# Kernel tuning notes

Hardware: AMD Instinct MI355X
Metric: run time of the kernel (lower is better)

The kernel has to match this reference:

```python
import jax, jax.numpy as jnp
import numpy as np

B, T, C = 2, 2048, 1024
H = 16
HD = C // H  # 64


def setup_inputs() -> dict:
    key = jax.random.key(0)
    k1, k2, k3, k4, k5 = jax.random.split(key, 5)
    s = 0.02
    return {
        "x": jax.random.normal(k1, (B, T, C), dtype=jnp.float32),
        "w_attn": jax.random.normal(k2, (C, 3 * C), dtype=jnp.float32) * s,
        "b_attn": jnp.zeros((3 * C,), dtype=jnp.float32),
        "w_proj": jax.random.normal(k3, (C, C), dtype=jnp.float32) * s,
        "b_proj": jnp.zeros((C,), dtype=jnp.float32),
    }


def reference(x, w_attn, b_attn, w_proj, b_proj):
    Bx, Tx, Cx = x.shape
    qkv = x @ w_attn + b_attn                      # [B,T,3C]
    q, k, v = jnp.split(qkv, 3, axis=-1)
    # [B,T,C] -> [B,H,T,HD]
    def heads(t):
        return t.reshape(Bx, Tx, H, HD).transpose(0, 2, 1, 3)
    q, k, v = heads(q), heads(k), heads(v)
    scale = 1.0 / np.sqrt(HD).astype(np.float32)
    scores = jnp.einsum("bhqd,bhkd->bhqk", q, k) * scale
    causal = jnp.tril(jnp.ones((Tx, Tx), dtype=bool))
    scores = jnp.where(causal, scores, -jnp.inf)
    attn = jax.nn.softmax(scores, axis=-1)          # dropout p=0 -> identity
    y = jnp.einsum("bhqk,bhkd->bhqd", attn, v)
    y = y.transpose(0, 2, 1, 3).reshape(Bx, Tx, Cx)
    return y @ w_proj + b_proj
```

## Files before the change

kernel.cpp:

```cpp
#include <hip/hip_runtime.h>
#include <hip/hip_bf16.h>

#define Bb 2
#define Tt 2048
#define Cc 1024
#define Hh 16
#define HD 64
#define QS 0.18033688f

typedef __attribute__((ext_vector_type(8))) short bf16x8;
typedef __attribute__((ext_vector_type(4))) short bf16x4;
typedef __attribute__((ext_vector_type(4))) float f32x4;
typedef __attribute__((ext_vector_type(2))) unsigned int u32x2;

__device__ inline short f2b(float f) {
    unsigned int u = __builtin_bit_cast(unsigned int, f);
    unsigned int r = (u + 0x7FFFu + ((u >> 16) & 1u)) >> 16;
    return (short)(unsigned short)r;
}

__device__ inline void gl16(const void* g, void* l) {
    __builtin_amdgcn_global_load_lds(
        (const __attribute__((address_space(1))) void*)g,
        (__attribute__((address_space(3))) void*)l, 16, 0, 0);
}

__global__ __launch_bounds__(256) void prep_kernel(
    const float* __restrict__ x, short* __restrict__ xbf,
    const float* __restrict__ wA, short* __restrict__ wAT,
    const float* __restrict__ wP, short* __restrict__ wPT)
{
    const int bx = blockIdx.x, tid = threadIdx.x;
    if (bx < 2048) {
        int i = (bx * 256 + tid) * 8;
        float4 a = *(const float4*)(x + i);
        float4 b = *(const float4*)(x + i + 4);
        bf16x8 v;
        v[0] = f2b(a.x); v[1] = f2b(a.y); v[2] = f2b(a.z); v[3] = f2b(a.w);
        v[4] = f2b(b.x); v[5] = f2b(b.y); v[6] = f2b(b.z); v[7] = f2b(b.w);
        *(bf16x8*)(xbf + i) = v;
        return;
    }
    const float* W; short* WT; int N, t;
    if (bx < 2816) { t = bx - 2048; W = wA; WT = wAT; N = 3072; }
    else           { t = bx - 2816; W = wP; WT = wPT; N = 1024; }
    const int K = 1024;
    int k0 = (t & 15) * 64, n0 = (t >> 4) * 64;
    int nl = tid & 63, kg = tid >> 6;
    int n = n0 + nl;
    short v[16];
#pragma unroll
    for (int i = 0; i < 16; i++)
        v[i] = f2b(W[(size_t)(k0 + kg * 16 + i) * N + n]);
    short* dst = WT + (size_t)n * K + k0 + kg * 16;
    *(bf16x8*)dst = *(bf16x8*)&v[0];
    *(bf16x8*)(dst + 8) = *(bf16x8*)&v[8];
}

#define VM4 asm volatile("s_waitcnt vmcnt(4)" ::: "memory")
#define VM2 asm volatile("s_waitcnt vmcnt(2)" ::: "memory")
#define VM0 asm volatile("s_waitcnt vmcnt(0)" ::: "memory")
#define VMN (void)0
#define BARRIER asm volatile("s_barrier" ::: "memory")

#define STG_A(nb, h, kb) { \
    gl16(A + baA[h] + (kb), &LB[(((nb) << 1) | (h)) * 8192 + dst8]); \
    gl16(A + baA[h] + 131072 + (kb), &LB[(((nb) << 1) | (h)) * 8192 + dst8 + 4096]); }
#define STG_B(nb, h, kb) { \
    gl16(Bt + baB[h] + (kb), &LB[32768 + (((nb) << 1) | (h)) * 8192 + dst8]); \
    gl16(Bt + baB[h] + 131072 + (kb), &LB[32768 + (((nb) << 1) | (h)) * 8192 + dst8 + 4096]); }

#define PHASE(bb, MH, NH, STG, WAIT) { \
    WAIT; \
    BARRIER; \
    const short* Ab_ = &LB[(((bb) << 1) | (MH)) * 8192]; \
    const short* Bb_ = &LB[32768 + (((bb) << 1) | (NH)) * 8192]; \
    bf16x8 af_[4][2], bf_[2][2]; \
    _Pragma("unroll") for (int f_ = 0; f_ < 4; f_++) \
        _Pragma("unroll") for (int kh_ = 0; kh_ < 2; kh_++) \
            af_[f_][kh_] = *(const bf16x8*)&Ab_[aro[f_] + kx[kh_]]; \
    _Pragma("unroll") for (int e_ = 0; e_ < 2; e_++) \
        _Pragma("unroll") for (int kh_ = 0; kh_ < 2; kh_++) \
            bf_[e_][kh_] = *(const bf16x8*)&Bb_[bro[e_] + kx[kh_]]; \
    STG; \
    __builtin_amdgcn_s_setprio(1); \
    _Pragma("unroll") for (int f_ = 0; f_ < 4; f_++) \
        _Pragma("unroll") for (int e_ = 0; e_ < 2; e_++) \
            _Pragma("unroll") for (int kh_ = 0; kh_ < 2; kh_++) \
                acc[(MH) * 4 + f_][(NH) * 2 + e_] = \
                    __builtin_amdgcn_mfma_f32_16x16x32_bf16( \
                        af_[f_][kh_], bf_[e_][kh_], \
                        acc[(MH) * 4 + f_][(NH) * 2 + e_], 0, 0, 0); \
    __builtin_amdgcn_s_setprio(0); }

__global__ __launch_bounds__(512, 2) void gemm_qkv(
    const short* __restrict__ A, const short* __restrict__ Bt,
    const float* __restrict__ bias,
    short* __restrict__ qw, short* __restrict__ kw, short* __restrict__ vTw,
    int M, int N, int K)
{
    __shared__ __attribute__((aligned(16))) short LB[65536];

    const int tid  = threadIdx.x;
    const int wave = tid >> 6, lane = tid & 63;
    const int quad = lane >> 4, lr = lane & 15;
    const int wm = wave >> 2, wn = wave & 3;

    const int bid = blockIdx.x;
    const int sw = (bid & 7) * 24 + (bid >> 3);
    const int bx = sw % 12, by = sw / 12;
    const int m0 = by * 256, n0 = bx * 256;

    const int dst8 = tid * 8;
    size_t baA[2], baB[2];
    {
        int r = tid >> 3;
        int cs = ((tid & 7) ^ (r & 7)) << 3;
#pragma unroll
        for (int h = 0; h < 2; h++) {
            int gA = m0 + ((r >> 6) << 7) + h * 64 + (r & 63);
            int gB = n0 + ((r >> 5) << 6) + h * 32 + (r & 31);
            baA[h] = (size_t)gA * 1024 + cs;
            baB[h] = (size_t)gB * 1024 + cs;
        }
    }

    int aro[4], bro[2], kx[2];
#pragma unroll
    for (int f = 0; f < 4; f++) aro[f] = (wm * 64 + f * 16 + lr) * 64;
#pragma unroll
    for (int e = 0; e < 2; e++) bro[e] = (wn * 32 + e * 16 + lr) * 64;
#pragma unroll
    for (int kh = 0; kh < 2; kh++)
        kx[kh] = (((kh * 4 + quad) ^ (lr & 7)) << 3);

    f32x4 acc[8][4];
    const f32x4 zf = {0.f, 0.f, 0.f, 0.f};
#pragma unroll
    for (int mf = 0; mf < 8; mf++)
#pragma unroll
        for (int nf = 0; nf < 4; nf++) acc[mf][nf] = zf;

    STG_A(0, 0, 0); STG_B(0, 0, 0); STG_A(0, 1, 0); STG_B(0, 1, 0);

    for (int t = 0; t < 15; ++t) {
        const int bb = t & 1, nb = bb ^ 1;
        const int kb1 = (t + 1) << 6;
        PHASE(bb, 0, 0, STG_A(nb, 0, kb1), VM4);
        PHASE(bb, 1, 0, STG_B(nb, 0, kb1), VM4);
        PHASE(bb, 0, 1, STG_A(nb, 1, kb1), VM4);
        PHASE(bb, 1, 1, STG_B(nb, 1, kb1), VMN);
    }
    PHASE(1, 0, 0, VMN, VM4);
    PHASE(1, 1, 0, VMN, VM2);
    PHASE(1, 0, 1, VMN, VM0);
    PHASE(1, 1, 1, VMN, VMN);

    if (n0 < 2048) {
#pragma unroll
        for (int nf = 0; nf < 4; nf++) {
            int c = n0 + wn * 64 + nf * 16 + lr;
            float bv = bias[c];
            int which = c >> 10, cc = c & 1023;
            int h = cc >> 6, d = cc & 63;
            short* base = which ? kw : qw;
            float qs = which ? 1.0f : QS;
#pragma unroll
            for (int mf = 0; mf < 8; mf++)
#pragma unroll
                for (int r = 0; r < 4; r++) {
                    int rg = m0 + wm * 128 + mf * 16 + quad * 4 + r;
                    int b = rg >> 11, tq = rg & 2047;
                    float val = acc[mf][nf][r] + bv;
                    base[(((size_t)b * Hh + h) * Tt + tq) * HD + d] = f2b(val * qs);
                }
        }
    } else {
#pragma unroll
        for (int p = 0; p < 2; p++) {
            __syncthreads();
            if ((wn >> 1) == p) {
#pragma unroll
                for (int nf = 0; nf < 4; nf++) {
                    int cl = (wn & 1) * 64 + nf * 16 + lr;
                    float bv = bias[n0 + p * 128 + cl];
#pragma unroll
                    for (int mf = 0; mf < 8; mf++)
#pragma unroll
                        for (int r = 0; r < 4; r++) {
                            int tl = wm * 128 + mf * 16 + quad * 4 + r;
                            LB[cl * 264 + tl] = f2b(acc[mf][nf][r] + bv);
                        }
                }
            }
            __syncthreads();
            const int rl = tid >> 2, seg = tid & 3;
            const int cc = (n0 & 1023) + p * 128 + rl;
            const int h = cc >> 6, d = cc & 63;
            const int b2 = m0 >> 11, tb = (m0 & 2047) + seg * 64;
            short* dstv = vTw + (((size_t)b2 * Hh + h) * HD + d) * Tt + tb;
            const short* srcv = &LB[rl * 264 + seg * 64];
#pragma unroll
            for (int jj = 0; jj < 8; jj++)
                *(bf16x8*)(dstv + jj * 8) = *(const bf16x8*)(srcv + jj * 8);
        }
    }
}

__global__ __launch_bounds__(256) void gemm_proj(
    const short* __restrict__ A, const short* __restrict__ Bt,
    const float* __restrict__ bias, float* __restrict__ out,
    int M, int N, int K)
{
    __shared__ __attribute__((aligned(16))) short SH[12288];

    const int tid  = threadIdx.x;
    const int wave = tid >> 6, lane = tid & 63;
    const int quad = lane >> 4, lr = lane & 15;
    const int wm = wave >> 1, wn = wave & 1;
    const int m0 = blockIdx.y * 64, n0 = blockIdx.x * 128;

    const int arow = tid >> 2;
    const int acol = ((tid & 3) ^ ((arow >> 1) & 3)) << 3;
    int brow[2], bcol[2];
#pragma unroll
    for (int i = 0; i < 2; i++) {
        int id = i * 256 + tid;
        brow[i] = id >> 2;
        bcol[i] = ((id & 3) ^ ((brow[i] >> 1) & 3)) << 3;
    }
    const int pfrag = quad ^ ((lr >> 1) & 3);

    f32x4 acc[2][4];
    const f32x4 zf = {0.f, 0.f, 0.f, 0.f};
#pragma unroll
    for (int mi = 0; mi < 2; mi++)
#pragma unroll
        for (int ni = 0; ni < 4; ni++) acc[mi][ni] = zf;

    auto asrc = [&](int row, int col) -> const short* {
        int rg = m0 + row, b = rg >> 11, t = rg & 2047;
        int h = col >> 6, d = col & 63;
        return A + ((((size_t)b * Hh + h) * Tt + t) * HD + d);
    };

    gl16(asrc(arow, acol), &SH[tid * 8]);
#pragma unroll
    for (int i = 0; i < 2; i++)
        gl16(Bt + (size_t)(n0 + brow[i]) * K + bcol[i],
             &SH[4096 + (i * 256 + tid) * 8]);

    const int iters = K >> 5;
    for (int it = 0; it < iters; ++it) {
        const int coA = (it & 1) * 2048, noA = ((it & 1) ^ 1) * 2048;
        const int coB = (it & 1) * 4096, noB = ((it & 1) ^ 1) * 4096;
        __syncthreads();
        if (it + 1 < iters) {
            const int k1 = (it + 1) << 5;
            gl16(asrc(arow, k1 + acol), &SH[noA + tid * 8]);
#pragma unroll
            for (int i = 0; i < 2; i++)
                gl16(Bt + (size_t)(n0 + brow[i]) * K + k1 + bcol[i],
                     &SH[4096 + noB + (i * 256 + tid) * 8]);
        }
        bf16x8 af[2], bf[4];
#pragma unroll
        for (int mi = 0; mi < 2; mi++) {
            int row = wm * 32 + mi * 16 + lr;
            af[mi] = *(bf16x8*)&SH[coA + (row * 4 + pfrag) * 8];
        }
#pragma unroll
        for (int ni = 0; ni < 4; ni++) {
            int row = wn * 64 + ni * 16 + lr;
            bf[ni] = *(bf16x8*)&SH[4096 + coB + (row * 4 + pfrag) * 8];
        }
#pragma unroll
        for (int mi = 0; mi < 2; mi++)
#pragma unroll
            for (int ni = 0; ni < 4; ni++)
                acc[mi][ni] = __builtin_amdgcn_mfma_f32_16x16x32_bf16(
                    af[mi], bf[ni], acc[mi][ni], 0, 0, 0);
    }

#pragma unroll
    for (int mi = 0; mi < 2; mi++)
#pragma unroll
        for (int ni = 0; ni < 4; ni++) {
            int c = n0 + wn * 64 + ni * 16 + lr;
            float bv = bias[c];
#pragma unroll
            for (int r = 0; r < 4; r++) {
                int rg = m0 + wm * 32 + mi * 16 + quad * 4 + r;
                out[(size_t)rg * N + c] = acc[mi][ni][r] + bv;
            }
        }
}

__global__ __launch_bounds__(256) void gemm_f32src(
    const void* __restrict__ Araw, const float* __restrict__ Bm,
    const float* __restrict__ bias, float* __restrict__ out,
    short* __restrict__ qw, short* __restrict__ kw, short* __restrict__ vTw,
    int M, int N, int K, int mode)
{
    __shared__ __attribute__((aligned(16))) short As[128 * 32];
    __shared__ __attribute__((aligned(16))) short Bs[128 * 32];

    const int tid  = threadIdx.x;
    const int wave = tid >> 6, lane = tid & 63;
    const int quad = lane >> 4, lr = lane & 15;
    const int wm = wave >> 1, wn = wave & 1;
    const int m0 = blockIdx.y * 128, n0 = blockIdx.x * 128;

    f32x4 acc[4][4];
    const f32x4 zf = {0.f, 0.f, 0.f, 0.f};
#pragma unroll
    for (int mi = 0; mi < 4; mi++)
#pragma unroll
        for (int ni = 0; ni < 4; ni++) acc[mi][ni] = zf;

    for (int k0 = 0; k0 < K; k0 += 32) {
        __syncthreads();
        if (mode == 1) {
            const float* Af = (const float*)Araw;
#pragma unroll
            for (int i = 0; i < 4; i++) {
                int id  = i * 256 + tid;
                int row = id >> 3;
                int kc  = (id & 7) << 2;
                float4 v = *(const float4*)(Af + (size_t)(m0 + row) * K + k0 + kc);
                short* d = &As[row * 32 + kc];
                d[0] = f2b(v.x); d[1] = f2b(v.y); d[2] = f2b(v.z); d[3] = f2b(v.w);
            }
        } else {
            const short* Ah = (const short*)Araw;
#pragma unroll
            for (int i = 0; i < 2; i++) {
                int id  = i * 256 + tid;
                int row = id >> 2;
                int kc  = (id & 3) << 3;
                int rg = m0 + row, b = rg >> 11, t = rg & 2047;
                int c = k0 + kc, h = c >> 6, d = c & 63;
                *(bf16x8*)&As[row * 32 + kc] =
                    *(const bf16x8*)(Ah + ((((size_t)b * Hh + h) * Tt + t) * HD + d));
            }
        }
#pragma unroll
        for (int i = 0; i < 4; i++) {
            int id = i * 256 + tid;
            int kr = id >> 5;
            int nc = (id & 31) << 2;
            float4 v = *(const float4*)(Bm + (size_t)(k0 + kr) * N + n0 + nc);
            Bs[(nc + 0) * 32 + kr] = f2b(v.x);
            Bs[(nc + 1) * 32 + kr] = f2b(v.y);
            Bs[(nc + 2) * 32 + kr] = f2b(v.z);
            Bs[(nc + 3) * 32 + kr] = f2b(v.w);
        }
        __syncthreads();

        bf16x8 af[4], bf[4];
#pragma unroll
        for (int mi = 0; mi < 4; mi++)
            af[mi] = *(bf16x8*)&As[(wm * 64 + mi * 16 + lr) * 32 + quad * 8];
#pragma unroll
        for (int ni = 0; ni < 4; ni++)
            bf[ni] = *(bf16x8*)&Bs[(wn * 64 + ni * 16 + lr) * 32 + quad * 8];
#pragma unroll
        for (int mi = 0; mi < 4; mi++)
#pragma unroll
            for (int ni = 0; ni < 4; ni++)
                acc[mi][ni] = __builtin_amdgcn_mfma_f32_16x16x32_bf16(
                    af[mi], bf[ni], acc[mi][ni], 0, 0, 0);
    }

#pragma unroll
    for (int mi = 0; mi < 4; mi++) {
#pragma unroll
        for (int ni = 0; ni < 4; ni++) {
            int c = n0 + wn * 64 + ni * 16 + lr;
            float bv = bias[c];
#pragma unroll
            for (int r = 0; r < 4; r++) {
                int rg = m0 + wm * 64 + mi * 16 + quad * 4 + r;
                float val = acc[mi][ni][r] + bv;
                if (mode == 1) {
                    int which = c >> 10, cc = c & 1023;
                    int h = cc >> 6, d = cc & 63;
                    int b = rg >> 11, t = rg & 2047;
                    size_t bh = (size_t)b * Hh + h;
                    if (which == 0)      qw[(bh * Tt + t) * HD + d] = f2b(val * QS);
                    else if (which == 1) kw[(bh * Tt + t) * HD + d] = f2b(val);
                    else                 vTw[(bh * HD + d) * Tt + t] = f2b(val);
                } else {
                    out[(size_t)rg * N + c] = val;
                }
            }
        }
    }
}

__global__ __launch_bounds__(256) void attn_kernel(
    short* __restrict__ qw, const short* __restrict__ kw,
    const short* __restrict__ vTw)
{
    __shared__ __attribute__((aligned(16))) short Ks[2][8192];
    __shared__ __attribute__((aligned(16))) short Vs[2][8192];

    const int bh = blockIdx.x & 31;
    const int g  = blockIdx.x >> 5;
    const int tid = threadIdx.x;
    const int wave = tid >> 6, lane = tid & 63;
    const int quad = lane >> 4, lr = lane & 15;

    const int pA = 2 * g + (wave >> 1);
    const int pB = 63 - pA;
    const int wh = (wave & 1) * 16;
    const int r0m[2] = { pA * 32 + wh, pB * 32 + wh };

    short* qp = qw + (size_t)bh * Tt * HD;
    const short* kp = kw + (size_t)bh * Tt * HD;
    const short* vp = vTw + (size_t)bh * HD * Tt;

    int krow[4], kcol[4], vrow[4], vcol[4];
#pragma unroll
    for (int i = 0; i < 4; i++) {
        int id = i * 256 + tid;
        krow[i] = id >> 3;
        kcol[i] = ((id & 7) ^ (krow[i] & 7)) << 3;
        vrow[i] = id >> 4;
        vcol[i] = ((id & 15) ^ (vrow[i] & 15)) << 3;
    }

    const int kb0b = lr * 64 + ((quad     ^ (lr & 7)) << 3);
    const int kb1b = lr * 64 + (((4 + quad) ^ (lr & 7)) << 3);
    const int qh = quad >> 1, ql = quad & 1;
    int vbase[4];
#pragma unroll
    for (int nt = 0; nt < 4; nt++)
        vbase[nt] = (nt * 16 + lr) * 128 + ql * 4;

    bf16x8 aq[2][2];
#pragma unroll
    for (int mt = 0; mt < 2; mt++)
#pragma unroll
        for (int h = 0; h < 2; h++)
            aq[mt][h] = *(const bf16x8*)(qp + (size_t)(r0m[mt] + lr) * HD
                                            + h * 32 + quad * 8);

    const f32x4 zf = {0.f, 0.f, 0.f, 0.f};
    f32x4 o[2][4];
    float lacc[2] = {0.f, 0.f};
#pragma unroll
    for (int mt = 0; mt < 2; mt++)
#pragma unroll
        for (int nt = 0; nt < 4; nt++) o[mt][nt] = zf;

#pragma unroll
    for (int i = 0; i < 4; i++) {
        gl16(kp + (size_t)krow[i] * HD + kcol[i], &Ks[0][(i * 256 + tid) * 8]);
        gl16(vp + (size_t)vrow[i] * Tt + vcol[i], &Vs[0][(i * 256 + tid) * 8]);
    }

    const int clast = ((63 - 2 * g) * 32 + 31) >> 7;
    for (int c = 0; c <= clast; ++c) {
        const int j0 = c << 7;
        const int cur = c & 1;
        __syncthreads();
        if (c < clast) {
#pragma unroll
            for (int i = 0; i < 4; i++) {
                gl16(kp + (size_t)(j0 + 128 + krow[i]) * HD + kcol[i],
                     &Ks[cur ^ 1][(i * 256 + tid) * 8]);
                gl16(vp + (size_t)vrow[i] * Tt + (j0 + 128) + vcol[i],
                     &Vs[cur ^ 1][(i * 256 + tid) * 8]);
            }
        }
        const short* Kc = &Ks[cur][0];
        const short* Vc = &Vs[cur][0];
        __builtin_amdgcn_s_setprio(1);
#pragma unroll
        for (int kt = 0; kt < 8; kt++) {
            const int k16 = j0 + kt * 16;
            const bool act0 = k16 <= r0m[0] + 15;
            const bool act1 = k16 <= r0m[1] + 15;
            if (!act1 && !act0) break;
            bf16x8 kb0 = *(const bf16x8*)&Kc[kt * 1024 + kb0b];
            bf16x8 kb1 = *(const bf16x8*)&Kc[kt * 1024 + kb1b];
            const int sl8 = (((kt * 2 + qh) ^ lr) << 3);
            bf16x4 va[4];
#pragma unroll
            for (int nt = 0; nt < 4; nt++)
                va[nt] = *(const bf16x4*)&Vc[vbase[nt] + sl8];
#pragma unroll
            for (int mt = 0; mt < 2; mt++) {
                if (!(mt ? act1 : act0)) continue;
                f32x4 s = __builtin_amdgcn_mfma_f32_16x16x32_bf16(
                    kb0, aq[mt][0], zf, 0, 0, 0);
                s = __builtin_amdgcn_mfma_f32_16x16x32_bf16(
                    kb1, aq[mt][1], s, 0, 0, 0);
                unsigned u[4];
                if (k16 + 15 <= r0m[mt]) {
#pragma unroll
                    for (int r = 0; r < 4; r++) {
                        float e = __builtin_amdgcn_exp2f(s[r]);
                        u[r] = __builtin_bit_cast(unsigned, e);
                        lacc[mt] += e;
                    }
                } else {
#pragma unroll
                    for (int r = 0; r < 4; r++) {
                        float e = __builtin_amdgcn_exp2f(s[r]);
                        if ((k16 + quad * 4 + r) > (r0m[mt] + lr)) e = 0.f;
                        u[r] = __builtin_bit_cast(unsigned, e);
                        lacc[mt] += e;
                    }
                }
                u32x2 pu = { __builtin_amdgcn_perm(u[1], u[0], 0x07060302u),
                             __builtin_amdgcn_perm(u[3], u[2], 0x07060302u) };
                bf16x4 pt = __builtin_bit_cast(bf16x4, pu);
#pragma unroll
                for (int nt = 0; nt < 4; nt++)
                    o[mt][nt] = __builtin_amdgcn_mfma_f32_16x16x16bf16_1k(
                        va[nt], pt, o[mt][nt], 0, 0, 0);
            }
        }
        __builtin_amdgcn_s_setprio(0);
    }

#pragma unroll
    for (int mt = 0; mt < 2; mt++) {
        lacc[mt] += __shfl_xor(lacc[mt], 16, 64);
        lacc[mt] += __shfl_xor(lacc[mt], 32, 64);
        lacc[mt] = 1.0f / lacc[mt];
    }

#pragma unroll
    for (int mt = 0; mt < 2; mt++)
#pragma unroll
        for (int nt = 0; nt < 4; nt++) {
            bf16x4 ov;
#pragma unroll
            for (int r = 0; r < 4; r++) ov[r] = f2b(o[mt][nt][r] * lacc[mt]);
            *(bf16x4*)(qp + (size_t)(r0m[mt] + lr) * HD + nt * 16 + quad * 4) = ov;
        }
}

extern "C" void kernel_launch(void* const* d_in, const int* in_sizes, int n_in,
                              void* d_out, int out_size, void* d_ws, size_t ws_size,
                              hipStream_t stream) {
    const float* x      = (const float*)d_in[0];
    const float* w_attn = (const float*)d_in[1];
    const float* b_attn = (const float*)d_in[2];
    const float* w_proj = (const float*)d_in[3];
    const float* b_proj = (const float*)d_in[4];
    float* out = (float*)d_out;

    const size_t per = (size_t)Bb * Hh * Tt * HD;
    short* qw  = (short*)d_ws;
    short* kw  = qw + per;
    short* vTw = kw + per;
    const int M = Bb * Tt;

    const size_t need_fast = (3 * per + per + (size_t)3072 * 1024 + (size_t)1024 * 1024) * 2;

    if (ws_size >= need_fast) {
        short* xbf = vTw + per;
        short* wAT = xbf + per;
        short* wPT = wAT + (size_t)3072 * 1024;

        prep_kernel<<<dim3(3072), 256, 0, stream>>>(x, xbf, w_attn, wAT, w_proj, wPT);

        gemm_qkv<<<dim3(192), 512, 0, stream>>>(
            xbf, wAT, b_attn, qw, kw, vTw, M, 3 * Cc, Cc);

        attn_kernel<<<dim3(512), 256, 0, stream>>>(qw, kw, vTw);

        gemm_proj<<<dim3(Cc / 128, M / 64), 256, 0, stream>>>(
            qw, wPT, b_proj, out, M, Cc, Cc);
    } else {
        gemm_f32src<<<dim3(3 * Cc / 128, M / 128), 256, 0, stream>>>(
            x, w_attn, b_attn, nullptr, qw, kw, vTw, M, 3 * Cc, Cc, 1);

        attn_kernel<<<dim3(512), 256, 0, stream>>>(qw, kw, vTw);

        gemm_f32src<<<dim3(Cc / 128, M / 128), 256, 0, stream>>>(
            qw, w_proj, b_proj, out, nullptr, nullptr, nullptr, M, Cc, Cc, 2);
    }
}
```

Before: 186.0 us.

## Restructure QKV GEMM main loop with serpentine quadrant order and prefetched B fragments

The QKV GEMM main loop is reorganised. It walks the four output quadrants in a snake order (00,01,11,10) so the B or A register fragments can be reused between consecutive quadrants. It also loads the next tile's first B fragment early, during the current tile. Sched barriers pin the order of LDS reads, global-to-LDS stages and MFMA blocks, and a second barrier per phase is added. This is meant to cut redundant LDS reads and hide LDS latency behind MFMAs, at the cost of more barriers, more fragment registers and stricter hand-tuned vmcnt accounting.

```diff
diff --git a/kernel.cpp b/kernel.cpp
--- a/kernel.cpp
+++ b/kernel.cpp
@@ -60,8 +60,8 @@
 #define VM4 asm volatile("s_waitcnt vmcnt(4)" ::: "memory")
 #define VM2 asm volatile("s_waitcnt vmcnt(2)" ::: "memory")
 #define VM0 asm volatile("s_waitcnt vmcnt(0)" ::: "memory")
-#define VMN (void)0
 #define BARRIER asm volatile("s_barrier" ::: "memory")
+#define SCHEDB __builtin_amdgcn_sched_barrier(0)
 
 #define STG_A(nb, h, kb) { \
     gl16(A + baA[h] + (kb), &LB[(((nb) << 1) | (h)) * 8192 + dst8]); \
@@ -70,28 +70,38 @@
     gl16(Bt + baB[h] + (kb), &LB[32768 + (((nb) << 1) | (h)) * 8192 + dst8]); \
     gl16(Bt + baB[h] + 131072 + (kb), &LB[32768 + (((nb) << 1) | (h)) * 8192 + dst8 + 4096]); }
 
-#define PHASE(bb, MH, NH, STG, WAIT) { \
-    WAIT; \
-    BARRIER; \
-    const short* Ab_ = &LB[(((bb) << 1) | (MH)) * 8192]; \
-    const short* Bb_ = &LB[32768 + (((bb) << 1) | (NH)) * 8192]; \
-    bf16x8 af_[4][2], bf_[2][2]; \
+#define RD_A(buf, h) { \
+    const short* Ab_ = &LB[(((buf) << 1) | (h)) * 8192]; \
     _Pragma("unroll") for (int f_ = 0; f_ < 4; f_++) \
         _Pragma("unroll") for (int kh_ = 0; kh_ < 2; kh_++) \
-            af_[f_][kh_] = *(const bf16x8*)&Ab_[aro[f_] + kx[kh_]]; \
+            bA[f_][kh_] = *(const bf16x8*)&Ab_[aro[f_] + kx[kh_]]; }
+
+#define RD_B(buf, h, dst) { \
+    const short* Bb_ = &LB[32768 + (((buf) << 1) | (h)) * 8192]; \
     _Pragma("unroll") for (int e_ = 0; e_ < 2; e_++) \
         _Pragma("unroll") for (int kh_ = 0; kh_ < 2; kh_++) \
-            bf_[e_][kh_] = *(const bf16x8*)&Bb_[bro[e_] + kx[kh_]]; \
-    STG; \
+            dst[e_][kh_] = *(const bf16x8*)&Bb_[bro[e_] + kx[kh_]]; }
+
+#define QMM(MH, NH, BR) { \
     __builtin_amdgcn_s_setprio(1); \
     _Pragma("unroll") for (int f_ = 0; f_ < 4; f_++) \
         _Pragma("unroll") for (int e_ = 0; e_ < 2; e_++) \
             _Pragma("unroll") for (int kh_ = 0; kh_ < 2; kh_++) \
                 acc[(MH) * 4 + f_][(NH) * 2 + e_] = \
                     __builtin_amdgcn_mfma_f32_16x16x32_bf16( \
-                        af_[f_][kh_], bf_[e_][kh_], \
+                        bA[f_][kh_], BR[e_][kh_], \
                         acc[(MH) * 4 + f_][(NH) * 2 + e_], 0, 0, 0); \
     __builtin_amdgcn_s_setprio(0); }
+
+#define TILE_FULL(bb, nb, kb1, B0C, B0N) { \
+    RD_A(bb, 0); STG_B(nb, 0, kb1); BARRIER; SCHEDB; \
+    QMM(0, 0, B0C); SCHEDB; VM4; BARRIER; \
+    RD_B(bb, 1, bB1); STG_A(nb, 0, kb1); BARRIER; SCHEDB; \
+    QMM(0, 1, bB1); SCHEDB; VM4; BARRIER; \
+    RD_A(bb, 1); STG_B(nb, 1, kb1); BARRIER; SCHEDB; \
+    QMM(1, 1, bB1); SCHEDB; VM4; BARRIER; \
+    RD_B(nb, 0, B0N); STG_A(nb, 1, kb1); BARRIER; SCHEDB; \
+    QMM(1, 0, B0C); SCHEDB; VM4; BARRIER; }
 
 __global__ __launch_bounds__(512, 2) void gemm_qkv(
     const short* __restrict__ A, const short* __restrict__ Bt,
@@ -141,20 +151,24 @@
 #pragma unroll
         for (int nf = 0; nf < 4; nf++) acc[mf][nf] = zf;
 
-    STG_A(0, 0, 0); STG_B(0, 0, 0); STG_A(0, 1, 0); STG_B(0, 1, 0);
-
-    for (int t = 0; t < 15; ++t) {
-        const int bb = t & 1, nb = bb ^ 1;
-        const int kb1 = (t + 1) << 6;
-        PHASE(bb, 0, 0, STG_A(nb, 0, kb1), VM4);
-        PHASE(bb, 1, 0, STG_B(nb, 0, kb1), VM4);
-        PHASE(bb, 0, 1, STG_A(nb, 1, kb1), VM4);
-        PHASE(bb, 1, 1, STG_B(nb, 1, kb1), VMN);
-    }
-    PHASE(1, 0, 0, VMN, VM4);
-    PHASE(1, 1, 0, VMN, VM2);
-    PHASE(1, 0, 1, VMN, VM0);
-    PHASE(1, 1, 1, VMN, VMN);
+    bf16x8 bA[4][2], bB1[2][2], B0x[2][2], B0y[2][2];
+
+    STG_B(0, 0, 0); STG_A(0, 0, 0); STG_B(0, 1, 0); STG_A(0, 1, 0);
+    VM4;
+    BARRIER;
+    RD_B(0, 0, B0x);
+
+    for (int it = 0; it < 7; ++it) {
+        const int kbe = (2 * it + 1) << 6;
+        const int kbo = (2 * it + 2) << 6;
+        TILE_FULL(0, 1, kbe, B0x, B0y);
+        TILE_FULL(1, 0, kbo, B0y, B0x);
+    }
+    TILE_FULL(0, 1, 15 << 6, B0x, B0y);
+    RD_A(1, 0); BARRIER; SCHEDB; QMM(0, 0, B0y); SCHEDB; VM2; BARRIER;
+    RD_B(1, 1, bB1); BARRIER; SCHEDB; QMM(0, 1, bB1); SCHEDB; VM0; BARRIER;
+    RD_A(1, 1); BARRIER; SCHEDB; QMM(1, 1, bB1); SCHEDB;
+    QMM(1, 0, B0y);
 
     if (n0 < 2048) {
 #pragma unroll
```

After: 184.8 us. Within noise of the previous version (-0.7%).
